# Performance work log

Measured on AMD Instinct MI355X. Metric: run time of the kernel, lower is better.

## Reference

```python
import jax, jax.numpy as jnp
import numpy as np

EMBED = 768
HEADS = 12
HEAD_DIM = EMBED // HEADS
HIDDEN = int(EMBED * 4.0)
EPS = 1e-5


def setup_inputs() -> dict:
    key = jax.random.key(0)
    ks = jax.random.split(key, 12)
    s = 0.02
    return {
        "x": jax.random.normal(ks[0], (8, 1024, EMBED), dtype=jnp.float32),
        # norm1 / norm2 (LayerNorm affine params)
        "g1": jnp.ones((EMBED,), jnp.float32),
        "b1": jnp.zeros((EMBED,), jnp.float32),
        "g2": jnp.ones((EMBED,), jnp.float32),
        "b2": jnp.zeros((EMBED,), jnp.float32),
        # attention weights (stored [in, out]; qkv_bias=False)
        "w_qkv": jax.random.normal(ks[1], (EMBED, 3 * EMBED), jnp.float32) * s,
        "w_proj": jax.random.normal(ks[2], (EMBED, EMBED), jnp.float32) * s,
        "b_proj": jnp.zeros((EMBED,), jnp.float32),
        # MLP weights
        "w_fc1": jax.random.normal(ks[3], (EMBED, HIDDEN), jnp.float32) * s,
        "b_fc1": jnp.zeros((HIDDEN,), jnp.float32),
        "w_fc2": jax.random.normal(ks[4], (HIDDEN, EMBED), jnp.float32) * s,
        "b_fc2": jnp.zeros((EMBED,), jnp.float32),
    }


def _layernorm(x, g, b):
    mu = jnp.mean(x, axis=-1, keepdims=True)
    var = jnp.var(x, axis=-1, keepdims=True)
    return (x - mu) * jax.lax.rsqrt(var + EPS) * g + b


def reference(x, g1, b1, g2, b2, w_qkv, w_proj, b_proj, w_fc1, b_fc1, w_fc2, b_fc2):
    B, N, C = x.shape
    scaling = HEAD_DIM ** (-0.5)

    # --- attention branch ---
    h = _layernorm(x, g1, b1)
    qkv = (h @ w_qkv).reshape(B, N, 3, HEADS, HEAD_DIM)
    q, k, v = qkv[:, :, 0], qkv[:, :, 1], qkv[:, :, 2]  # [B, N, H, D]
    attn = jnp.einsum("bnhd,bmhd->bhnm", q, k) * scaling  # full NxN scores
    attn = jax.nn.softmax(attn, axis=-1)
    out = jnp.einsum("bhnm,bmhd->bnhd", attn, v).reshape(B, N, C)
    out = out @ w_proj + b_proj
    x = x + out

    # --- MLP branch ---
    h = _layernorm(x, g2, b2)
    h = jax.nn.gelu(h @ w_fc1 + b_fc1, approximate=False)
    h = h @ w_fc2 + b_fc2
    return x + h
```

## Files before the change

### kernel.cpp

```cpp
#include <hip/hip_runtime.h>
#include <hip/hip_bf16.h>
#include <math.h>

#define EMBED 768
#define HEADS 12
#define HEAD_DIM 64
#define HIDDEN 3072
#define SEQ 1024
#define BATCH 8
#define TOKENS (SEQ*BATCH)

typedef unsigned short u16;
typedef __attribute__((ext_vector_type(8))) short bf16x8;
typedef __attribute__((ext_vector_type(4))) float floatx4;
typedef __attribute__((ext_vector_type(4))) u16 u16x4;
typedef __attribute__((ext_vector_type(2))) u16 u16x2;

__device__ __forceinline__ u16 f2bf(float f){
    union { float f; unsigned u; } v; v.f = f;
    unsigned r = v.u + 0x7fffu + ((v.u >> 16) & 1u);
    return (u16)(r >> 16);
}

__device__ __forceinline__ void gload16(const void* g, void* l){
    __builtin_amdgcn_global_load_lds((const __attribute__((address_space(1))) void*)g,
                                     (__attribute__((address_space(3))) void*)l, 16, 0, 0);
}

__device__ __forceinline__ float gelu_fast(float x){
    float t = 1.5957691216f * (x + 0.044715f * x * x * x);
    return x / (1.0f + __expf(-t));
}

__global__ __launch_bounds__(256) void prep_kernel(const float* __restrict__ w0, const float* __restrict__ w1,
                                   const float* __restrict__ w2, const float* __restrict__ w3,
                                   u16* __restrict__ o0, u16* __restrict__ o1,
                                   u16* __restrict__ o2, u16* __restrict__ o3,
                                   const float* __restrict__ x, const float* __restrict__ g,
                                   const float* __restrict__ bln, u16* __restrict__ lnout){
    int bb = blockIdx.x;
    int tid = threadIdx.x;
    if(bb >= 6912){
        int row  = (bb - 6912) * 4 + (tid >> 6);
        int lane = tid & 63;
        const float4* xr = (const float4*)(x + (size_t)row * EMBED);
        float4 v[3];
        float s = 0.f;
        #pragma unroll
        for(int i=0;i<3;i++){
            v[i] = xr[i*64 + lane];
            s += v[i].x + v[i].y + v[i].z + v[i].w;
        }
        #pragma unroll
        for(int o=32;o>0;o>>=1) s += __shfl_xor(s, o);
        float mu = s * (1.0f/EMBED);
        float s2 = 0.f;
        #pragma unroll
        for(int i=0;i<3;i++){
            float dx = v[i].x-mu, dy = v[i].y-mu, dz = v[i].z-mu, dw = v[i].w-mu;
            s2 += dx*dx + dy*dy + dz*dz + dw*dw;
        }
        #pragma unroll
        for(int o=32;o>0;o>>=1) s2 += __shfl_xor(s2, o);
        float rstd = rsqrtf(s2*(1.0f/EMBED) + 1e-5f);
        u16* orow = lnout + (size_t)row * EMBED;
        const float4* g4 = (const float4*)g;
        const float4* b4 = (const float4*)bln;
        #pragma unroll
        for(int i=0;i<3;i++){
            int c4 = i*64 + lane;
            float4 gv = g4[c4], bv = b4[c4];
            u16x4 pk;
            pk.x = f2bf((v[i].x-mu)*rstd*gv.x + bv.x);
            pk.y = f2bf((v[i].y-mu)*rstd*gv.y + bv.y);
            pk.z = f2bf((v[i].z-mu)*rstd*gv.z + bv.z);
            pk.w = f2bf((v[i].w-mu)*rstd*gv.w + bv.w);
            *(u16x4*)(orow + c4*4) = pk;
        }
        return;
    }
    const float* W; u16* Wt; int K, N, bx, by;
    if(bb < 1728)      { int l = bb;        W=w0; Wt=o0; K=768;  N=2304; bx=l%72; by=l/72; }
    else if(bb < 2304) { int l = bb-1728;   W=w1; Wt=o1; K=768;  N=768;  bx=l%24; by=l/24; }
    else if(bb < 4608) { int l = bb-2304;   W=w2; Wt=o2; K=768;  N=3072; bx=l%96; by=l/96; }
    else               { int l = bb-4608;   W=w3; Wt=o3; K=3072; N=768;  bx=l%24; by=l/24; }

    __shared__ float tile[32][33];
    int n0 = bx * 32, k0 = by * 32;
    int tx = tid & 31, ty = tid >> 5;
    #pragma unroll
    for(int i=0;i<32;i+=8) tile[ty+i][tx] = W[(size_t)(k0+ty+i)*N + n0+tx];
    __syncthreads();
    int kp = (tid & 15)*2, nn = tid >> 4;
    #pragma unroll
    for(int p=0;p<2;p++){
        int n = nn + p*16;
        u16x2 w2v;
        w2v.x = f2bf(tile[kp  ][n]);
        w2v.y = f2bf(tile[kp+1][n]);
        *(u16x2*)(Wt + (size_t)(n0+n)*K + k0 + kp) = w2v;
    }
}

__global__ __launch_bounds__(256) void ln_kernel(const float* __restrict__ x, const float* __restrict__ g,
                                                 const float* __restrict__ b, u16* __restrict__ out){
    int row  = blockIdx.x * 4 + (threadIdx.x >> 6);
    int lane = threadIdx.x & 63;
    const float4* xr = (const float4*)(x + (size_t)row * EMBED);
    float4 v[3];
    float s = 0.f;
    #pragma unroll
    for(int i=0;i<3;i++){
        v[i] = xr[i*64 + lane];
        s += v[i].x + v[i].y + v[i].z + v[i].w;
    }
    #pragma unroll
    for(int o=32;o>0;o>>=1) s += __shfl_xor(s, o);
    float mu = s * (1.0f/EMBED);
    float s2 = 0.f;
    #pragma unroll
    for(int i=0;i<3;i++){
        float dx = v[i].x-mu, dy = v[i].y-mu, dz = v[i].z-mu, dw = v[i].w-mu;
        s2 += dx*dx + dy*dy + dz*dz + dw*dw;
    }
    #pragma unroll
    for(int o=32;o>0;o>>=1) s2 += __shfl_xor(s2, o);
    float rstd = rsqrtf(s2*(1.0f/EMBED) + 1e-5f);
    u16* orow = out + (size_t)row * EMBED;
    const float4* g4 = (const float4*)g;
    const float4* b4 = (const float4*)b;
    #pragma unroll
    for(int i=0;i<3;i++){
        int c4 = i*64 + lane;
        float4 gv = g4[c4], bv = b4[c4];
        u16x4 pk;
        pk.x = f2bf((v[i].x-mu)*rstd*gv.x + bv.x);
        pk.y = f2bf((v[i].y-mu)*rstd*gv.y + bv.y);
        pk.z = f2bf((v[i].z-mu)*rstd*gv.z + bv.z);
        pk.w = f2bf((v[i].w-mu)*rstd*gv.w + bv.w);
        *(u16x4*)(orow + c4*4) = pk;
    }
}

template<int EPI>
__global__ __launch_bounds__(512,4) void gemm_wide(const u16* __restrict__ A, const u16* __restrict__ Bt,
        void* __restrict__ Cout, const float* __restrict__ bias, const float* __restrict__ res,
        u16* __restrict__ vt, int M, int N, int K, int ldc){
    __shared__ __align__(16) u16 As[128*64];
    __shared__ __align__(16) u16 Bs[256*64];
    int tid  = threadIdx.x;
    int wave = tid >> 6, lane = tid & 63;
    int quad = lane >> 4, lm = lane & 15;
    int wm = (wave >> 2) * 64;
    int wn = (wave & 3) * 64;

    int gx = gridDim.x;
    int bid = blockIdx.y * gx + blockIdx.x;
    int nwg = gx * gridDim.y;
    int cpx = nwg >> 3;
    int swz = (bid & 7) * cpx + (bid >> 3);
    int m0 = (swz / gx) * 128, n0 = (swz % gx) * 256;

    floatx4 acc[4][4];
    #pragma unroll
    for(int i=0;i<4;i++)
        #pragma unroll
        for(int j=0;j<4;j++) acc[i][j] = (floatx4){0.f,0.f,0.f,0.f};

    int srow = tid >> 3;
    int scol = ((tid & 7) ^ (srow & 7)) * 8;
    const u16* aP[2];
    const u16* bP[4];
    #pragma unroll
    for(int p=0;p<2;p++) aP[p] = A  + (size_t)(m0 + p*64 + srow) * K + scol;
    #pragma unroll
    for(int p=0;p<4;p++) bP[p] = Bt + (size_t)(n0 + p*64 + srow) * K + scol;

    for(int k0=0; k0<K; k0+=64){
        __syncthreads();
        #pragma unroll
        for(int p=0;p<2;p++) gload16(aP[p] + k0, As + p*4096 + tid*8);
        #pragma unroll
        for(int p=0;p<4;p++) gload16(bP[p] + k0, Bs + p*4096 + tid*8);
        __syncthreads();
        #pragma unroll
        for(int ks=0;ks<2;ks++){
            int slotoff = (((ks*4+quad) ^ (lm&7)) << 3);
            bf16x8 af[4], bfr[4];
            #pragma unroll
            for(int i=0;i<4;i++)
                af[i]  = *(const bf16x8*)(As + (wm + i*16 + lm)*64 + slotoff);
            #pragma unroll
            for(int i=0;i<4;i++)
                bfr[i] = *(const bf16x8*)(Bs + (wn + i*16 + lm)*64 + slotoff);
            #pragma unroll
            for(int mf=0;mf<4;mf++)
                #pragma unroll
                for(int nf=0;nf<4;nf++)
                    acc[mf][nf] = __builtin_amdgcn_mfma_f32_16x16x32_bf16(af[mf], bfr[nf], acc[mf][nf], 0, 0, 0);
        }
    }

    if(EPI == 3 && n0 >= 1536){
        #pragma unroll
        for(int nf=0;nf<4;nf++){
            int col = n0 + wn + nf*16 + lm;
            int hh = (col - 1536) >> 6;
            int d  = col & 63;
            #pragma unroll
            for(int mf=0;mf<4;mf++){
                int row0 = m0 + wm + mf*16 + quad*4;
                int bb  = row0 >> 10;
                int key = row0 & 1023;
                u16x4 pk;
                #pragma unroll
                for(int r=0;r<4;r++) pk[r] = f2bf(acc[mf][nf][r]);
                *(u16x4*)(vt + ((size_t)(bb*HEADS+hh)*64 + d)*SEQ + key) = pk;
            }
        }
        return;
    }

    #pragma unroll
    for(int nf=0;nf<4;nf++){
        int col = n0 + wn + nf*16 + lm;
        float bv = bias ? bias[col] : 0.f;
        #pragma unroll
        for(int mf=0;mf<4;mf++){
            int row0 = m0 + wm + mf*16 + quad*4;
            #pragma unroll
            for(int r=0;r<4;r++){
                float v = acc[mf][nf][r] + bv;
                size_t idx = (size_t)(row0 + r) * ldc + col;
                if(EPI == 1){
                    v = gelu_fast(v);
                    ((u16*)Cout)[idx] = f2bf(v);
                } else {
                    ((u16*)Cout)[idx] = f2bf(v);
                }
            }
        }
    }
}

template<int EPI, int BM>
__global__ __launch_bounds__(256) void gemm_bt(const u16* __restrict__ A, const u16* __restrict__ Bt,
        void* __restrict__ Cout, const float* __restrict__ bias, const float* __restrict__ res,
        u16* __restrict__ vt, int M, int N, int K, int ldc){
    constexpr int MF = BM/32;
    __shared__ __align__(16) u16 As[BM*64];
    __shared__ __align__(16) u16 Bs[128*64];
    int tid  = threadIdx.x;
    int wave = tid >> 6, lane = tid & 63;
    int quad = lane >> 4, lm = lane & 15;

    int gx = gridDim.x;
    int bid = blockIdx.y * gx + blockIdx.x;
    int nwg = gx * gridDim.y;
    int cpx = nwg >> 3;
    int swz = (bid & 7) * cpx + (bid >> 3);
    int m0 = (swz / gx) * BM, n0 = (swz % gx) * 128;

    int wm = (wave & 1) * (BM/2);
    int wn = (wave >> 1) * 64;

    floatx4 acc[MF][4];
    #pragma unroll
    for(int i=0;i<MF;i++)
        #pragma unroll
        for(int j=0;j<4;j++) acc[i][j] = (floatx4){0.f,0.f,0.f,0.f};

    int srow = tid >> 3;
    int scol = ((tid & 7) ^ (srow & 7)) * 8;
    const u16* aP[MF];
    const u16* bP[4];
    #pragma unroll
    for(int p=0;p<MF;p++) aP[p] = A  + (size_t)(m0 + p*32 + srow) * K + scol;
    #pragma unroll
    for(int p=0;p<4;p++)  bP[p] = Bt + (size_t)(n0 + p*32 + srow) * K + scol;

    for(int k0=0; k0<K; k0+=64){
        __syncthreads();
        #pragma unroll
        for(int p=0;p<MF;p++) gload16(aP[p] + k0, As + p*2048 + tid*8);
        #pragma unroll
        for(int p=0;p<4;p++)  gload16(bP[p] + k0, Bs + p*2048 + tid*8);
        __syncthreads();
        #pragma unroll
        for(int ks=0;ks<2;ks++){
            int slotoff = (((ks*4+quad) ^ (lm&7)) << 3);
            bf16x8 af[MF], bfr[4];
            #pragma unroll
            for(int i=0;i<MF;i++)
                af[i]  = *(const bf16x8*)(As + (wm + i*16 + lm)*64 + slotoff);
            #pragma unroll
            for(int i=0;i<4;i++)
                bfr[i] = *(const bf16x8*)(Bs + (wn + i*16 + lm)*64 + slotoff);
            #pragma unroll
            for(int mf=0;mf<MF;mf++)
                #pragma unroll
                for(int nf=0;nf<4;nf++)
                    acc[mf][nf] = __builtin_amdgcn_mfma_f32_16x16x32_bf16(af[mf], bfr[nf], acc[mf][nf], 0, 0, 0);
        }
    }

    #pragma unroll
    for(int nf=0;nf<4;nf++){
        int col = n0 + wn + nf*16 + lm;
        float bv = bias ? bias[col] : 0.f;
        #pragma unroll
        for(int mf=0;mf<MF;mf++){
            int row0 = m0 + wm + mf*16 + quad*4;
            #pragma unroll
            for(int r=0;r<4;r++){
                float v = acc[mf][nf][r] + bv;
                size_t idx = (size_t)(row0 + r) * ldc + col;
                if(EPI == 2){
                    ((float*)Cout)[idx] = v + res[idx];
                } else {
                    ((u16*)Cout)[idx] = f2bf(v);
                }
            }
        }
    }
}

__global__ __launch_bounds__(256) void attn_kernel(const u16* __restrict__ qk, const u16* __restrict__ vt,
                                                   u16* __restrict__ out){
    int qt = blockIdx.x, h = blockIdx.y, b = blockIdx.z;
    int tid = threadIdx.x;
    int wave = tid >> 6, lane = tid & 63;
    int quad = lane >> 4, lm = lane & 15;

    __shared__ __align__(16) u16 Ks[2*64*64];
    __shared__ __align__(16) u16 Vs[2*64*64];
    __shared__ __align__(16) u16 P[4*32*64];

    const u16* qbase = qk + (size_t)b * SEQ * 1536;
    const u16* vbase = vt + (size_t)(b*HEADS + h) * 64 * SEQ;
    u16* Pw = P + wave*2048;

    int q0 = qt*128 + wave*32;
    bf16x8 qf[2][2];
    #pragma unroll
    for(int qi=0;qi<2;qi++){
        const u16* qp = qbase + (size_t)(q0 + qi*16 + lm)*1536 + h*64;
        qf[qi][0] = *(const bf16x8*)(qp + quad*8);
        qf[qi][1] = *(const bf16x8*)(qp + 32 + quad*8);
    }

    float l_i[2] = {0.f, 0.f};
    floatx4 o_acc[2][4];
    #pragma unroll
    for(int qi=0;qi<2;qi++)
        #pragma unroll
        for(int nf=0;nf<4;nf++) o_acc[qi][nf] = (floatx4){0.f,0.f,0.f,0.f};

    int sr = lane >> 3;
    int sp = lane & 7;
    const float C = 0.18033688011112186f;

    auto stage = [&](int kt, int buf){
        #pragma unroll
        for(int i=0;i<2;i++){
            int rr = wave*16 + i*8 + sr;
            int sw = (sp ^ (rr & 7)) * 8;
            gload16(qbase + (size_t)(kt*64 + rr)*1536 + 768 + h*64 + sw,
                    Ks + buf*4096 + (wave*16 + i*8)*64 + lane*8);
            gload16(vbase + (size_t)rr*SEQ + kt*64 + sw,
                    Vs + buf*4096 + (wave*16 + i*8)*64 + lane*8);
        }
    };

    stage(0, 0);
    __syncthreads();

    int cur = 0;
    for(int kt=0; kt<16; kt++){
        if(kt < 15) stage(kt+1, cur^1);
        const u16* Ksb = Ks + cur*4096;
        const u16* Vsb = Vs + cur*4096;

        floatx4 s[4][2];
        #pragma unroll
        for(int kf=0;kf<4;kf++){
            int krow = kf*16 + lm;
            bf16x8 k0 = *(const bf16x8*)(Ksb + krow*64 + ((quad     ^ (lm&7))*8));
            bf16x8 k1 = *(const bf16x8*)(Ksb + krow*64 + (((4+quad) ^ (lm&7))*8));
            #pragma unroll
            for(int qi=0;qi<2;qi++){
                floatx4 t = (floatx4){0.f,0.f,0.f,0.f};
                t = __builtin_amdgcn_mfma_f32_16x16x32_bf16(k0, qf[qi][0], t, 0, 0, 0);
                t = __builtin_amdgcn_mfma_f32_16x16x32_bf16(k1, qf[qi][1], t, 0, 0, 0);
                s[kf][qi] = t;
            }
        }

        #pragma unroll
        for(int qi=0;qi<2;qi++){
            float part = 0.f;
            #pragma unroll
            for(int kf=0;kf<4;kf++){
                #pragma unroll
                for(int r=0;r<4;r++){
                    float e = exp2f(s[kf][qi][r]*C);
                    s[kf][qi][r] = e;
                    part += e;
                }
            }
            part += __shfl_xor(part, 16);
            part += __shfl_xor(part, 32);
            l_i[qi] += part;
            #pragma unroll
            for(int kf=0;kf<4;kf++){
                u16x4 pk;
                #pragma unroll
                for(int r=0;r<4;r++) pk[r] = f2bf(s[kf][qi][r]);
                int c  = kf*4 + quad;
                int cp = c ^ (2*(lm & 7));
                *(u16x4*)(Pw + (qi*16 + lm)*64 + cp*4) = pk;
            }
        }

        #pragma unroll
        for(int ks=0;ks<2;ks++){
            bf16x8 vf[4];
            #pragma unroll
            for(int nf=0;nf<4;nf++)
                vf[nf] = *(const bf16x8*)(Vsb + (nf*16+lm)*64 + (((ks*4+quad) ^ (lm&7))*8));
            #pragma unroll
            for(int qi=0;qi<2;qi++){
                int cr = (ks*8 + 2*quad) ^ (2*(lm & 7));
                bf16x8 pa = *(const bf16x8*)(Pw + (qi*16 + lm)*64 + cr*4);
                #pragma unroll
                for(int nf=0;nf<4;nf++)
                    o_acc[qi][nf] = __builtin_amdgcn_mfma_f32_16x16x32_bf16(pa, vf[nf], o_acc[qi][nf], 0, 0, 0);
            }
        }
        if(kt < 15) __syncthreads();
        cur ^= 1;
    }

    #pragma unroll
    for(int qi=0;qi<2;qi++){
        float rl[4];
        #pragma unroll
        for(int r=0;r<4;r++) rl[r] = 1.0f / __shfl(l_i[qi], quad*4 + r);
        int token = b*SEQ + qt*128 + wave*32 + qi*16 + quad*4;
        #pragma unroll
        for(int nf=0;nf<4;nf++){
            #pragma unroll
            for(int r=0;r<4;r++){
                out[(size_t)(token + r)*EMBED + h*64 + nf*16 + lm] = f2bf(o_acc[qi][nf][r] * rl[r]);
            }
        }
    }
}

extern "C" void kernel_launch(void* const* d_in, const int* in_sizes, int n_in,
                              void* d_out, int out_size, void* d_ws, size_t ws_size,
                              hipStream_t stream) {
    const float* x      = (const float*)d_in[0];
    const float* g1     = (const float*)d_in[1];
    const float* b1     = (const float*)d_in[2];
    const float* g2     = (const float*)d_in[3];
    const float* b2     = (const float*)d_in[4];
    const float* w_qkv  = (const float*)d_in[5];
    const float* w_proj = (const float*)d_in[6];
    const float* b_proj = (const float*)d_in[7];
    const float* w_fc1  = (const float*)d_in[8];
    const float* b_fc1  = (const float*)d_in[9];
    const float* w_fc2  = (const float*)d_in[10];
    const float* b_fc2  = (const float*)d_in[11];
    float* out = (float*)d_out;

    char* ws = (char*)d_ws;
    u16*   wqkv_t  = (u16*)  (ws + 0);
    u16*   wproj_t = (u16*)  (ws + 3538944);
    u16*   wfc1_t  = (u16*)  (ws + 4718592);
    u16*   wfc2_t  = (u16*)  (ws + 9437184);
    float* x1      = (float*)(ws + 14155776);
    u16*   hbuf    = (u16*)  (ws + 39321600);
    u16*   qkbuf   = (u16*)  (ws + 51904512);
    u16*   vtbuf   = (u16*)  (ws + 77070336);
    u16*   attn_o  = (u16*)  (ws + 89653248);
    u16*   fc1_o   = qkbuf;
    u16*   h2      = hbuf;

    prep_kernel<<<8960, 256, 0, stream>>>(w_qkv, w_proj, w_fc1, w_fc2,
                                          wqkv_t, wproj_t, wfc1_t, wfc2_t,
                                          x, g1, b1, hbuf);

    gemm_wide<3><<<dim3(2304/256, TOKENS/128), 512, 0, stream>>>(hbuf, wqkv_t, qkbuf, nullptr, nullptr, vtbuf, TOKENS, 2304, 768, 1536);

    attn_kernel<<<dim3(8, HEADS, BATCH), 256, 0, stream>>>(qkbuf, vtbuf, attn_o);

    gemm_bt<2,64><<<dim3( 768/128, TOKENS/64), 256, 0, stream>>>(attn_o, wproj_t, x1, b_proj, x, nullptr, TOKENS, 768, 768, 768);

    ln_kernel<<<TOKENS/4, 256, 0, stream>>>(x1, g2, b2, h2);

    gemm_wide<1><<<dim3(3072/256, TOKENS/128), 512, 0, stream>>>(h2, wfc1_t, fc1_o, b_fc1, nullptr, nullptr, TOKENS, 3072, 768, 3072);

    gemm_bt<2,64><<<dim3( 768/128, TOKENS/64), 256, 0, stream>>>(fc1_o, wfc2_t, out, b_fc2, x1, nullptr, TOKENS, 768, 3072, 768);
}
```

Baseline: 348.9 us.

## Double-buffer GEMM B tiles with async prefetch and reorder attention grid

Both GEMM kernels now keep two LDS buffers for the B (weight) tile and prefetch the next K-slice of B while computing on the current one. Explicit vmcnt waits and raw s_barrier calls replace the two __syncthreads per iteration. The attention launch becomes a 1D grid ordered so that blocks sharing a query tile across heads and batches are adjacent. Epilogue loops are reordered to write row-major. The larger LDS footprint may reduce occupancy. The A tile is still single-buffered, and the hand-placed waitcnt counts depend on the exact number of gload16 calls issued.

```diff
diff --git a/kernel.cpp b/kernel.cpp
--- a/kernel.cpp
+++ b/kernel.cpp
@@ -147,7 +147,7 @@
         void* __restrict__ Cout, const float* __restrict__ bias, const float* __restrict__ res,
         u16* __restrict__ vt, int M, int N, int K, int ldc){
     __shared__ __align__(16) u16 As[128*64];
-    __shared__ __align__(16) u16 Bs[256*64];
+    __shared__ __align__(16) u16 Bs[2*256*64];
     int tid  = threadIdx.x;
     int wave = tid >> 6, lane = tid & 63;
     int quad = lane >> 4, lm = lane & 15;
@@ -176,13 +176,24 @@
     #pragma unroll
     for(int p=0;p<4;p++) bP[p] = Bt + (size_t)(n0 + p*64 + srow) * K + scol;
 
-    for(int k0=0; k0<K; k0+=64){
-        __syncthreads();
+    int nt = K / 64;
+    #pragma unroll
+    for(int p=0;p<4;p++) gload16(bP[p], Bs + p*4096 + tid*8);
+
+    for(int t=0; t<nt; ++t){
+        int cur = t & 1, nxt = cur ^ 1;
+        size_t k0 = (size_t)t * 64;
         #pragma unroll
         for(int p=0;p<2;p++) gload16(aP[p] + k0, As + p*4096 + tid*8);
-        #pragma unroll
-        for(int p=0;p<4;p++) gload16(bP[p] + k0, Bs + p*4096 + tid*8);
-        __syncthreads();
+        if(t+1 < nt){
+            #pragma unroll
+            for(int p=0;p<4;p++) gload16(bP[p] + k0 + 64, Bs + nxt*16384 + p*4096 + tid*8);
+            asm volatile("s_waitcnt vmcnt(4)" ::: "memory");
+        } else {
+            asm volatile("s_waitcnt vmcnt(0)" ::: "memory");
+        }
+        __builtin_amdgcn_s_barrier();
+        const u16* Bc = Bs + cur*16384;
         #pragma unroll
         for(int ks=0;ks<2;ks++){
             int slotoff = (((ks*4+quad) ^ (lm&7)) << 3);
@@ -192,13 +203,14 @@
                 af[i]  = *(const bf16x8*)(As + (wm + i*16 + lm)*64 + slotoff);
             #pragma unroll
             for(int i=0;i<4;i++)
-                bfr[i] = *(const bf16x8*)(Bs + (wn + i*16 + lm)*64 + slotoff);
+                bfr[i] = *(const bf16x8*)(Bc + (wn + i*16 + lm)*64 + slotoff);
             #pragma unroll
             for(int mf=0;mf<4;mf++)
                 #pragma unroll
                 for(int nf=0;nf<4;nf++)
                     acc[mf][nf] = __builtin_amdgcn_mfma_f32_16x16x32_bf16(af[mf], bfr[nf], acc[mf][nf], 0, 0, 0);
         }
+        __builtin_amdgcn_s_barrier();
     }
 
     if(EPI == 3 && n0 >= 1536){
@@ -221,23 +233,21 @@
         return;
     }
 
-    #pragma unroll
-    for(int nf=0;nf<4;nf++){
-        int col = n0 + wn + nf*16 + lm;
-        float bv = bias ? bias[col] : 0.f;
-        #pragma unroll
-        for(int mf=0;mf<4;mf++){
-            int row0 = m0 + wm + mf*16 + quad*4;
-            #pragma unroll
-            for(int r=0;r<4;r++){
-                float v = acc[mf][nf][r] + bv;
-                size_t idx = (size_t)(row0 + r) * ldc + col;
-                if(EPI == 1){
-                    v = gelu_fast(v);
-                    ((u16*)Cout)[idx] = f2bf(v);
-                } else {
-                    ((u16*)Cout)[idx] = f2bf(v);
-                }
+    float bvv[4];
+    #pragma unroll
+    for(int nf=0;nf<4;nf++) bvv[nf] = bias ? bias[n0 + wn + nf*16 + lm] : 0.f;
+    #pragma unroll
+    for(int mf=0;mf<4;mf++){
+        int row0 = m0 + wm + mf*16 + quad*4;
+        #pragma unroll
+        for(int r=0;r<4;r++){
+            size_t rowoff = (size_t)(row0 + r) * ldc;
+            #pragma unroll
+            for(int nf=0;nf<4;nf++){
+                int col = n0 + wn + nf*16 + lm;
+                float v = acc[mf][nf][r] + bvv[nf];
+                if(EPI == 1) v = gelu_fast(v);
+                ((u16*)Cout)[rowoff + col] = f2bf(v);
             }
         }
     }
@@ -249,7 +259,7 @@
         u16* __restrict__ vt, int M, int N, int K, int ldc){
     constexpr int MF = BM/32;
     __shared__ __align__(16) u16 As[BM*64];
-    __shared__ __align__(16) u16 Bs[128*64];
+    __shared__ __align__(16) u16 Bs[2*128*64];
     int tid  = threadIdx.x;
     int wave = tid >> 6, lane = tid & 63;
     int quad = lane >> 4, lm = lane & 15;
@@ -279,13 +289,24 @@
     #pragma unroll
     for(int p=0;p<4;p++)  bP[p] = Bt + (size_t)(n0 + p*32 + srow) * K + scol;
 
-    for(int k0=0; k0<K; k0+=64){
-        __syncthreads();
+    int nt = K / 64;
+    #pragma unroll
+    for(int p=0;p<4;p++) gload16(bP[p], Bs + p*2048 + tid*8);
+
+    for(int t=0; t<nt; ++t){
+        int cur = t & 1, nxt = cur ^ 1;
+        size_t k0 = (size_t)t * 64;
         #pragma unroll
         for(int p=0;p<MF;p++) gload16(aP[p] + k0, As + p*2048 + tid*8);
-        #pragma unroll
-        for(int p=0;p<4;p++)  gload16(bP[p] + k0, Bs + p*2048 + tid*8);
-        __syncthreads();
+        if(t+1 < nt){
+            #pragma unroll
+            for(int p=0;p<4;p++) gload16(bP[p] + k0 + 64, Bs + nxt*8192 + p*2048 + tid*8);
+            asm volatile("s_waitcnt vmcnt(4)" ::: "memory");
+        } else {
+            asm volatile("s_waitcnt vmcnt(0)" ::: "memory");
+        }
+        __builtin_amdgcn_s_barrier();
+        const u16* Bc = Bs + cur*8192;
         #pragma unroll
         for(int ks=0;ks<2;ks++){
             int slotoff = (((ks*4+quad) ^ (lm&7)) << 3);
@@ -295,30 +316,33 @@
                 af[i]  = *(const bf16x8*)(As + (wm + i*16 + lm)*64 + slotoff);
             #pragma unroll
             for(int i=0;i<4;i++)
-                bfr[i] = *(const bf16x8*)(Bs + (wn + i*16 + lm)*64 + slotoff);
+                bfr[i] = *(const bf16x8*)(Bc + (wn + i*16 + lm)*64 + slotoff);
             #pragma unroll
             for(int mf=0;mf<MF;mf++)
                 #pragma unroll
                 for(int nf=0;nf<4;nf++)
                     acc[mf][nf] = __builtin_amdgcn_mfma_f32_16x16x32_bf16(af[mf], bfr[nf], acc[mf][nf], 0, 0, 0);
         }
-    }
-
-    #pragma unroll
-    for(int nf=0;nf<4;nf++){
-        int col = n0 + wn + nf*16 + lm;
-        float bv = bias ? bias[col] : 0.f;
-        #pragma unroll
-        for(int mf=0;mf<MF;mf++){
-            int row0 = m0 + wm + mf*16 + quad*4;
-            #pragma unroll
-            for(int r=0;r<4;r++){
-                float v = acc[mf][nf][r] + bv;
-                size_t idx = (size_t)(row0 + r) * ldc + col;
+        __builtin_amdgcn_s_barrier();
+    }
+
+    float bvv[4];
+    #pragma unroll
+    for(int nf=0;nf<4;nf++) bvv[nf] = bias ? bias[n0 + wn + nf*16 + lm] : 0.f;
+    #pragma unroll
+    for(int mf=0;mf<MF;mf++){
+        int row0 = m0 + wm + mf*16 + quad*4;
+        #pragma unroll
+        for(int r=0;r<4;r++){
+            size_t rowoff = (size_t)(row0 + r) * ldc;
+            #pragma unroll
+            for(int nf=0;nf<4;nf++){
+                int col = n0 + wn + nf*16 + lm;
+                float v = acc[mf][nf][r] + bvv[nf];
                 if(EPI == 2){
-                    ((float*)Cout)[idx] = v + res[idx];
+                    ((float*)Cout)[rowoff + col] = v + res[rowoff + col];
                 } else {
-                    ((u16*)Cout)[idx] = f2bf(v);
+                    ((u16*)Cout)[rowoff + col] = f2bf(v);
                 }
             }
         }
@@ -327,7 +351,10 @@
 
 __global__ __launch_bounds__(256) void attn_kernel(const u16* __restrict__ qk, const u16* __restrict__ vt,
                                                    u16* __restrict__ out){
-    int qt = blockIdx.x, h = blockIdx.y, b = blockIdx.z;
+    int bid = blockIdx.x;
+    int hb = bid % 96;
+    int qt = bid / 96;
+    int h = hb % HEADS, b = hb / HEADS;
     int tid = threadIdx.x;
     int wave = tid >> 6, lane = tid & 63;
     int quad = lane >> 4, lm = lane & 15;
@@ -448,10 +475,11 @@
         for(int r=0;r<4;r++) rl[r] = 1.0f / __shfl(l_i[qi], quad*4 + r);
         int token = b*SEQ + qt*128 + wave*32 + qi*16 + quad*4;
         #pragma unroll
-        for(int nf=0;nf<4;nf++){
-            #pragma unroll
-            for(int r=0;r<4;r++){
-                out[(size_t)(token + r)*EMBED + h*64 + nf*16 + lm] = f2bf(o_acc[qi][nf][r] * rl[r]);
+        for(int r=0;r<4;r++){
+            size_t rowoff = (size_t)(token + r)*EMBED + h*64;
+            #pragma unroll
+            for(int nf=0;nf<4;nf++){
+                out[rowoff + nf*16 + lm] = f2bf(o_acc[qi][nf][r] * rl[r]);
             }
         }
     }
@@ -493,7 +521,7 @@
 
     gemm_wide<3><<<dim3(2304/256, TOKENS/128), 512, 0, stream>>>(hbuf, wqkv_t, qkbuf, nullptr, nullptr, vtbuf, TOKENS, 2304, 768, 1536);
 
-    attn_kernel<<<dim3(8, HEADS, BATCH), 256, 0, stream>>>(qkbuf, vtbuf, attn_o);
+    attn_kernel<<<768, 256, 0, stream>>>(qkbuf, vtbuf, attn_o);
 
     gemm_bt<2,64><<<dim3( 768/128, TOKENS/64), 256, 0, stream>>>(attn_o, wproj_t, x1, b_proj, x, nullptr, TOKENS, 768, 768, 768);
 
```

After: 344.9 us. Within noise of the previous version (-1.1%).
